# Optimization experiments

Hardware: AMD Instinct MI355X
Metric: run time of the kernel (lower is better)

The kernel has to match this reference:

```python
import jax, jax.numpy as jnp
import numpy as np

D_MODEL = 1024
NUM_HEADS = 16
HEAD_DIM = D_MODEL // NUM_HEADS


def setup_inputs() -> dict:
    key = jax.random.key(0)
    k_x, k_wqkv, k_bqkv, k_wfc, k_bfc = jax.random.split(key, 5)
    scale_in = 1.0 / np.sqrt(D_MODEL)
    return {
        "x": jax.random.normal(k_x, (2, 2048, D_MODEL), dtype=jnp.float32),
        # torch nn.Linear stores weight as [out_features, in_features]
        "w_qkv": jax.random.uniform(k_wqkv, (3 * D_MODEL, D_MODEL), jnp.float32, -scale_in, scale_in),
        "b_qkv": jax.random.uniform(k_bqkv, (3 * D_MODEL,), jnp.float32, -scale_in, scale_in),
        "w_fc": jax.random.uniform(k_wfc, (D_MODEL, D_MODEL), jnp.float32, -scale_in, scale_in),
        "b_fc": jax.random.uniform(k_bfc, (D_MODEL,), jnp.float32, -scale_in, scale_in),
    }


def reference(x, w_qkv, b_qkv, w_fc, b_fc):
    B, S, _ = x.shape
    # fused QKV projection: [B,S,3*d_model]
    qkv = jnp.einsum("bsd,ed->bse", x, w_qkv) + b_qkv
    # [B,S,H,3*head_dim] -> [B,H,S,3*head_dim]
    qkv = qkv.reshape(B, S, NUM_HEADS, 3 * HEAD_DIM).transpose(0, 2, 1, 3)
    Q, K, V = jnp.split(qkv, 3, axis=-1)  # each [B,H,S,head_dim]
    scores = jnp.einsum("bhqd,bhkd->bhqk", Q, K) / np.sqrt(HEAD_DIM).astype(np.float32)
    attention = jax.nn.softmax(scores, axis=-1)  # [B,H,S,S]
    values = jnp.einsum("bhqk,bhkd->bhqd", attention, V)
    # [B,H,S,head_dim] -> [B,S,d_model]
    values = values.transpose(0, 2, 1, 3).reshape(B, S, D_MODEL)
    out = jnp.einsum("bsd,ed->bse", values, w_fc) + b_fc
    return out
```

## Files before the change

### kernel.cpp

```cpp
#include <hip/hip_runtime.h>
#include <hip/hip_bf16.h>
#include <hip/hip_fp16.h>

#define D_MODEL 1024
#define NH 16
#define HD 64
#define BATCH 2
#define SEQ 2048

typedef __attribute__((ext_vector_type(8))) short short8;
typedef __attribute__((ext_vector_type(4))) float floatx4;
typedef __attribute__((ext_vector_type(16))) float floatx16;
typedef __attribute__((ext_vector_type(8))) _Float16 half8;

static __device__ __forceinline__ short f2bf(float f) {
    __hip_bfloat16 h = __float2bfloat16(f);
    return *reinterpret_cast<short*>(&h);
}
static __device__ __forceinline__ unsigned int pk2bf(float a, float b) {
    float2 t; t.x = a; t.y = b;
    __hip_bfloat162 h2 = __float22bfloat162_rn(t);
    return *reinterpret_cast<unsigned int*>(&h2);
}
static __device__ __forceinline__ void pl32swap(unsigned &a, unsigned &b) {
    asm("v_permlane32_swap_b32 %0, %1" : "+v"(a), "+v"(b));
}
static __device__ __forceinline__ short8 mk8(unsigned a, unsigned b,
                                             unsigned c, unsigned d) {
    union { unsigned u[4]; short8 s; } t;
    t.u[0] = a; t.u[1] = b; t.u[2] = c; t.u[3] = d;
    return t.s;
}

#define GLDS(gp, lp) __builtin_amdgcn_global_load_lds( \
    (const __attribute__((address_space(1))) void*)(gp), \
    (__attribute__((address_space(3))) void*)(lp), 16, 0, 0)

__global__ __launch_bounds__(256) void cvt_all(
    const float* __restrict__ x, const float* __restrict__ wq,
    const float* __restrict__ wf,
    short* __restrict__ Xb, short* __restrict__ Wqb, short* __restrict__ Wfb)
{
    int i = blockIdx.x * 256 + threadIdx.x;
    const float* src; short* dst; int off;
    if (i < 524288)      { src = x;  dst = Xb;  off = i; }
    else if (i < 917504) { src = wq; dst = Wqb; off = i - 524288; }
    else                 { src = wf; dst = Wfb; off = i - 917504; }
    float4 a = *reinterpret_cast<const float4*>(src + off * 8);
    float4 b = *reinterpret_cast<const float4*>(src + off * 8 + 4);
    short8 o;
    o[0] = f2bf(a.x); o[1] = f2bf(a.y); o[2] = f2bf(a.z); o[3] = f2bf(a.w);
    o[4] = f2bf(b.x); o[5] = f2bf(b.y); o[6] = f2bf(b.z); o[7] = f2bf(b.w);
    *reinterpret_cast<short8*>(dst + off * 8) = o;
}

__global__ __launch_bounds__(256) void qkv_gemm(
    const short* __restrict__ X, const short* __restrict__ W,
    const float* __restrict__ bias,
    short* __restrict__ Qs, short* __restrict__ Ks, short* __restrict__ Vt_g)
{
    __shared__ __align__(16) short As[128 * 128];
    __shared__ __align__(16) short Bs[128 * 128];
    const int tid = threadIdx.x;

    const int lin = blockIdx.x;
    const int g = lin & 7;
    const int loc = lin >> 3;
    const int mi = loc / 3;
    const int j3 = loc - mi * 3;
    const int m0 = mi * 128;
    const int n0 = (g + 8 * j3) * 128;
    const int bi = m0 >> 11, sl0 = m0 & 2047;

    const int w = tid >> 6, lane = tid & 63;
    const int quad = lane >> 4, l15 = lane & 15;
    const int wm2 = w >> 1, wn2 = w & 1;

    const int rg = lane >> 3;
    const int sl = lane & 7;
    const int cg = sl ^ rg;

    floatx4 acc[4][4];
#pragma unroll
    for (int i = 0; i < 4; i++)
#pragma unroll
        for (int j = 0; j < 4; j++) acc[i][j] = (floatx4)0.0f;

    for (int k0 = 0; k0 < 1024; k0 += 128) {
        __syncthreads();
#pragma unroll
        for (int jj = 0; jj < 4; jj++) {
            int grp = w * 4 + jj;
            int r = grp * 8 + rg;
#pragma unroll
            for (int kh = 0; kh < 2; kh++) {
                GLDS(&X[(size_t)(m0 + r) * 1024 + k0 + kh * 64 + cg * 8],
                     &As[grp * 1024 + kh * 512]);
                GLDS(&W[(size_t)(n0 + r) * 1024 + k0 + kh * 64 + cg * 8],
                     &Bs[grp * 1024 + kh * 512]);
            }
        }
        __syncthreads();
#pragma unroll
        for (int kk = 0; kk < 4; kk++) {
            const int kw = kk * 32 + quad * 8;
            const int base = (kw >> 6) * 512 +
                             ((((kw & 63) >> 3) ^ (l15 & 7)) * 8);
            short8 a[4], b[4];
#pragma unroll
            for (int t = 0; t < 4; t++) {
                int ra = wm2 * 64 + t * 16 + l15;
                int rb = wn2 * 64 + t * 16 + l15;
                a[t] = *reinterpret_cast<const short8*>(
                    &As[(ra >> 3) * 1024 + (ra & 7) * 64 + base]);
                b[t] = *reinterpret_cast<const short8*>(
                    &Bs[(rb >> 3) * 1024 + (rb & 7) * 64 + base]);
            }
#pragma unroll
            for (int mt = 0; mt < 4; mt++)
#pragma unroll
                for (int nt = 0; nt < 4; nt++)
                    acc[mt][nt] = __builtin_amdgcn_mfma_f32_16x16x32_bf16(
                        a[mt], b[nt], acc[mt][nt], 0, 0, 0);
        }
    }

    __syncthreads();
    short* EA = &As[0];
    short* T  = &As[0];
#pragma unroll
    for (int half = 0; half < 2; half++) {
        const int colg0 = n0 + half * 64;
        const int h = colg0 / 192;
        const int t = (colg0 % 192) / 64;
        if (wn2 == half) {
#pragma unroll
            for (int nt = 0; nt < 4; nt++) {
                int jj = nt * 16 + l15;
                float bv = bias[colg0 + jj];
#pragma unroll
                for (int mt = 0; mt < 4; mt++) {
#pragma unroll
                    for (int r = 0; r < 4; r++) {
                        int ml = wm2 * 64 + mt * 16 + quad * 4 + r;
                        float v = acc[mt][nt][r] + bv;
                        if (t == 0) v *= 0.18033688f;
                        if (t < 2) EA[ml * 72 + jj] = f2bf(v);
                        else       T[jj * 136 + ml] = f2bf(v);
                    }
                }
            }
        }
        __syncthreads();
        if (t < 2) {
            short* dst = (t == 0) ? Qs : Ks;
#pragma unroll
            for (int i = 0; i < 4; i++) {
                int c = tid + i * 256;
                int row = c >> 3, ck = c & 7;
                uint4 u = *reinterpret_cast<const uint4*>(&EA[row * 72 + ck * 8]);
                *reinterpret_cast<uint4*>(
                    &dst[((size_t)(bi * NH + h) * SEQ + sl0 + row) * HD + ck * 8]) = u;
            }
        } else {
#pragma unroll
            for (int i = 0; i < 4; i++) {
                int c = tid + i * 256;
                int d = c >> 4, ck = c & 15;
                uint4 u = *reinterpret_cast<const uint4*>(&T[d * 136 + ck * 8]);
                *reinterpret_cast<uint4*>(
                    &Vt_g[((size_t)(bi * NH + h) * HD + d) * SEQ + sl0 + ck * 8]) = u;
            }
        }
        __syncthreads();
    }
}

__global__ __launch_bounds__(256, 2) void attn_kernel(
    const short* __restrict__ Qs, const short* __restrict__ Ks,
    const short* __restrict__ Vt_g,
    _Float16* __restrict__ Opart, float* __restrict__ lpart)
{
    __shared__ __align__(16) short Kl[2][32 * 64];
    __shared__ __align__(16) short Vl[2][32 * 64];

    const int tid = threadIdx.x;
    const int w = tid >> 6, lane = tid & 63;
    const int hi = lane >> 5, l31 = lane & 31;

    const int lin = blockIdx.x;
    const int xcd = lin & 7;
    const int j = lin >> 3;
    const int qb = j & 7;
    const int grp = xcd + 8 * (j >> 3);
    const int khalf = grp & 1;
    const int h = (grp >> 1) & 15;
    const int bi = grp >> 5;
    const int bh = bi * NH + h;
    const int kbase = bh * SEQ * HD;
    const int vbase = bh * HD * SEQ;
    const int kt0 = khalf * (SEQ / 2);
    const int qw = qb * 256 + w * 64;

    const int sr = tid >> 3;
    const int ss = tid & 7;
    const int cgs = ss ^ (sr & 7);
    const short* kg = Ks + kbase + (size_t)(kt0 + sr) * HD + cgs * 8;
    const short* vg = Vt_g + vbase +
                      (size_t)(sr + (cgs >> 2) * 32) * SEQ + kt0 + (cgs & 3) * 8;

    const short8 onesv = {(short)0x3F80, (short)0x3F80, (short)0x3F80, (short)0x3F80,
                          (short)0x3F80, (short)0x3F80, (short)0x3F80, (short)0x3F80};

    short8 aq[2][4];
#pragma unroll
    for (int qt = 0; qt < 2; qt++) {
        const short* qp = Qs + kbase + (size_t)(qw + qt * 32 + l31) * HD + hi * 8;
#pragma unroll
        for (int c = 0; c < 4; c++)
            aq[qt][c] = *reinterpret_cast<const short8*>(qp + c * 16);
    }

    floatx16 o[2][2], ol[2];
#pragma unroll
    for (int qt = 0; qt < 2; qt++) {
        ol[qt] = (floatx16)0.0f;
        o[qt][0] = (floatx16)0.0f;
        o[qt][1] = (floatx16)0.0f;
    }

    const int rbase = (l31 >> 3) * 512 + (l31 & 7) * 64;
    const int rx = l31 & 7;

    GLDS(kg, &Kl[0][tid * 8]);
    GLDS(vg, &Vl[0][tid * 8]);
    __syncthreads();

    int cur = 0;
    for (int it = 0; it < SEQ / 2 / 32; it++) {
        GLDS(kg + (size_t)(it + 1) * (32 * HD), &Kl[cur ^ 1][tid * 8]);
        GLDS(vg + (it + 1) * 32, &Vl[cur ^ 1][tid * 8]);

        const short* Kb = &Kl[cur][0];
        const short* Vb = &Vl[cur][0];
        short8 kf[4], vA0, vA1, vB0, vB1;
#pragma unroll
        for (int c = 0; c < 4; c++)
            kf[c] = *reinterpret_cast<const short8*>(
                Kb + rbase + (((2 * c + hi) ^ rx) * 8));
        vA0 = *reinterpret_cast<const short8*>(Vb + rbase + (((0 + hi) ^ rx) * 8));
        vA1 = *reinterpret_cast<const short8*>(Vb + rbase + (((2 + hi) ^ rx) * 8));
        vB0 = *reinterpret_cast<const short8*>(Vb + rbase + (((4 + hi) ^ rx) * 8));
        vB1 = *reinterpret_cast<const short8*>(Vb + rbase + (((6 + hi) ^ rx) * 8));

#pragma unroll
        for (int qt = 0; qt < 2; qt++) {
            floatx16 s = (floatx16)0.0f;
            s = __builtin_amdgcn_mfma_f32_32x32x16_bf16(kf[0], aq[qt][0], s, 0, 0, 0);
            s = __builtin_amdgcn_mfma_f32_32x32x16_bf16(kf[1], aq[qt][1], s, 0, 0, 0);
            s = __builtin_amdgcn_mfma_f32_32x32x16_bf16(kf[2], aq[qt][2], s, 0, 0, 0);
            s = __builtin_amdgcn_mfma_f32_32x32x16_bf16(kf[3], aq[qt][3], s, 0, 0, 0);

            float p[16];
#pragma unroll
            for (int r = 0; r < 16; r++) p[r] = exp2f(s[r]);

            unsigned d0a = pk2bf(p[0], p[1]),   d2a = pk2bf(p[4], p[5]);
            unsigned d1a = pk2bf(p[2], p[3]),   d3a = pk2bf(p[6], p[7]);
            pl32swap(d0a, d2a);
            pl32swap(d1a, d3a);
            unsigned d0b = pk2bf(p[8], p[9]),   d2b = pk2bf(p[12], p[13]);
            unsigned d1b = pk2bf(p[10], p[11]), d3b = pk2bf(p[14], p[15]);
            pl32swap(d0b, d2b);
            pl32swap(d1b, d3b);
            short8 pa0 = mk8(d0a, d1a, d2a, d3a);
            short8 pa1 = mk8(d0b, d1b, d2b, d3b);

            o[qt][0] = __builtin_amdgcn_mfma_f32_32x32x16_bf16(pa0, vA0, o[qt][0], 0, 0, 0);
            o[qt][1] = __builtin_amdgcn_mfma_f32_32x32x16_bf16(pa0, vB0, o[qt][1], 0, 0, 0);
            o[qt][0] = __builtin_amdgcn_mfma_f32_32x32x16_bf16(pa1, vA1, o[qt][0], 0, 0, 0);
            o[qt][1] = __builtin_amdgcn_mfma_f32_32x32x16_bf16(pa1, vB1, o[qt][1], 0, 0, 0);
            ol[qt] = __builtin_amdgcn_mfma_f32_32x32x16_bf16(pa0, onesv, ol[qt], 0, 0, 0);
            ol[qt] = __builtin_amdgcn_mfma_f32_32x32x16_bf16(pa1, onesv, ol[qt], 0, 0, 0);
        }

        __syncthreads();
        cur ^= 1;
    }

#pragma unroll
    for (int qt = 0; qt < 2; qt++) {
#pragma unroll
        for (int r = 0; r < 16; r++) {
            int ql = qw + qt * 32 + (r & 3) + 8 * (r >> 2) + 4 * hi;
            size_t base = (size_t)khalf * (4096u * 1024u) +
                          ((size_t)bi * SEQ + ql) * D_MODEL + h * HD;
            Opart[base + l31]      = (_Float16)o[qt][0][r];
            Opart[base + 32 + l31] = (_Float16)o[qt][1][r];
            if (l31 == 0)
                lpart[khalf * 65536 + bh * SEQ + ql] = ol[qt][r];
        }
    }
}

__global__ __launch_bounds__(256) void combine_kernel(
    const _Float16* __restrict__ O, const float* __restrict__ lp,
    short* __restrict__ attnb)
{
    int i = blockIdx.x * 256 + threadIdx.x;
    int m = i >> 7;
    int e0 = (i & 127) * 8;
    int bi = m >> 11, s = m & 2047, h = e0 >> 6;
    int bh = bi * NH + h;
    float l = lp[bh * SEQ + s] + lp[65536 + bh * SEQ + s];
    float rl = 1.0f / l;
    size_t off = (size_t)m * D_MODEL + e0;
    half8 a = *reinterpret_cast<const half8*>(O + off);
    half8 b = *reinterpret_cast<const half8*>(O + 4096u * 1024u + off);
    short8 out;
#pragma unroll
    for (int j = 0; j < 8; j++)
        out[j] = f2bf(((float)a[j] + (float)b[j]) * rl);
    *reinterpret_cast<short8*>(attnb + off) = out;
}

__global__ __launch_bounds__(256) void fc_gemm(
    const short* __restrict__ A, const short* __restrict__ W,
    const float* __restrict__ bias, float* __restrict__ out)
{
    __shared__ __align__(16) short As[128 * 64];
    __shared__ __align__(16) short Bs[64 * 64];
    const int tid = threadIdx.x;
    const int m0 = blockIdx.y * 128;
    const int n0 = blockIdx.x * 64;
    const int w = tid >> 6, lane = tid & 63;
    const int quad = lane >> 4, l15 = lane & 15;
    const int wm2 = w >> 1, wn2 = w & 1;

    const int rg = lane >> 3;
    const int sl = lane & 7;
    const int cg = sl ^ rg;

    floatx4 acc[4][2];
#pragma unroll
    for (int i = 0; i < 4; i++)
#pragma unroll
        for (int j = 0; j < 2; j++) acc[i][j] = (floatx4)0.0f;

    for (int k0 = 0; k0 < 1024; k0 += 64) {
        __syncthreads();
#pragma unroll
        for (int j = 0; j < 4; j++) {
            int g = w * 4 + j;
            int r = g * 8 + rg;
            GLDS(&A[(size_t)(m0 + r) * 1024 + k0 + cg * 8], &As[g * 512]);
        }
#pragma unroll
        for (int j = 0; j < 2; j++) {
            int g = w * 2 + j;
            int r = g * 8 + rg;
            GLDS(&W[(size_t)(n0 + r) * 1024 + k0 + cg * 8], &Bs[g * 512]);
        }
        __syncthreads();
#pragma unroll
        for (int kk = 0; kk < 2; kk++) {
            int swz = ((kk * 4 + quad) ^ (l15 & 7)) * 8;
            short8 a[4], b[2];
#pragma unroll
            for (int i = 0; i < 4; i++)
                a[i] = *reinterpret_cast<const short8*>(
                    &As[(wm2 * 64 + i * 16 + l15) * 64 + swz]);
#pragma unroll
            for (int j = 0; j < 2; j++)
                b[j] = *reinterpret_cast<const short8*>(
                    &Bs[(wn2 * 32 + j * 16 + l15) * 64 + swz]);
#pragma unroll
            for (int mt = 0; mt < 4; mt++)
#pragma unroll
                for (int nt = 0; nt < 2; nt++)
                    acc[mt][nt] = __builtin_amdgcn_mfma_f32_16x16x32_bf16(
                        a[mt], b[nt], acc[mt][nt], 0, 0, 0);
        }
    }

#pragma unroll
    for (int nt = 0; nt < 2; nt++) {
        int col = n0 + wn2 * 32 + nt * 16 + l15;
        float bv = bias[col];
#pragma unroll
        for (int mt = 0; mt < 4; mt++) {
#pragma unroll
            for (int r = 0; r < 4; r++) {
                int row = m0 + wm2 * 64 + mt * 16 + quad * 4 + r;
                out[row * 1024 + col] = acc[mt][nt][r] + bv;
            }
        }
    }
}

extern "C" void kernel_launch(void* const* d_in, const int* in_sizes, int n_in,
                              void* d_out, int out_size, void* d_ws, size_t ws_size,
                              hipStream_t stream) {
    const float* x     = (const float*)d_in[0];
    const float* w_qkv = (const float*)d_in[1];
    const float* b_qkv = (const float*)d_in[2];
    const float* w_fc  = (const float*)d_in[3];
    const float* b_fc  = (const float*)d_in[4];
    float* out = (float*)d_out;

    const size_t M1 = 1024u * 1024u;
    short* ws = (short*)d_ws;
    short* Qs    = ws;
    short* Ks    = ws + 4 * M1;
    short* Vt_g  = ws + 8 * M1;
    short* Wfb   = ws + 12 * M1;
    short* Xb    = ws + 13 * M1;
    short* Wqb   = ws + 17 * M1;
    _Float16* Opart = (_Float16*)(ws + 13 * M1);
    float* lpart = (float*)(ws + 21 * M1);
    short* attnb = Qs;

    cvt_all<<<4096, 256, 0, stream>>>(x, w_qkv, w_fc, Xb, Wqb, Wfb);
    qkv_gemm<<<768, 256, 0, stream>>>(Xb, Wqb, b_qkv, Qs, Ks, Vt_g);
    attn_kernel<<<512, 256, 0, stream>>>(Qs, Ks, Vt_g, Opart, lpart);
    combine_kernel<<<2048, 256, 0, stream>>>(Opart, lpart, attnb);
    fc_gemm<<<dim3(16, 32), 256, 0, stream>>>(attnb, Wfb, b_fc, out);
}
```

Before: 214.5 us.

## Use 8 waves per attention block with one query tile each, sum rowsums on VALU

The attention kernel now launches 512 threads per block, with each wave handling one 32-row query tile instead of two. The K and V staging loads are split between the two halves of the block. The softmax row-sum is now accumulated with VALU adds plus a cross-half shuffle, replacing the extra MFMA against a ones vector. This cuts per-wave register pressure to allow more resident waves and removes two MFMAs per tile. In exchange, each wave now reuses the K/V fragments it reads from LDS for only one query tile.

Measured after the change: 213.7 us. About the same (-0.4%).

```diff
diff --git a/kernel.cpp b/kernel.cpp
--- a/kernel.cpp
+++ b/kernel.cpp
@@ -176,7 +176,7 @@
     }
 }
 
-__global__ __launch_bounds__(256, 2) void attn_kernel(
+__global__ __launch_bounds__(512, 4) void attn_kernel(
     const short* __restrict__ Qs, const short* __restrict__ Ks,
     const short* __restrict__ Vt_g,
     _Float16* __restrict__ Opart, float* __restrict__ lpart)
@@ -185,7 +185,8 @@
     __shared__ __align__(16) short Vl[2][32 * 64];
 
     const int tid = threadIdx.x;
-    const int w = tid >> 6, lane = tid & 63;
+    const int w = tid >> 6;
+    const int lane = tid & 63;
     const int hi = lane >> 5, l31 = lane & 31;
 
     const int lin = blockIdx.x;
@@ -200,46 +201,38 @@
     const int kbase = bh * SEQ * HD;
     const int vbase = bh * HD * SEQ;
     const int kt0 = khalf * (SEQ / 2);
-    const int qw = qb * 256 + w * 64;
-
-    const int sr = tid >> 3;
-    const int ss = tid & 7;
+    const int qw = qb * 256 + w * 32;
+
+    const int st = tid & 255;
+    const int sr = st >> 3;
+    const int ss = st & 7;
     const int cgs = ss ^ (sr & 7);
     const short* kg = Ks + kbase + (size_t)(kt0 + sr) * HD + cgs * 8;
     const short* vg = Vt_g + vbase +
                       (size_t)(sr + (cgs >> 2) * 32) * SEQ + kt0 + (cgs & 3) * 8;
 
-    const short8 onesv = {(short)0x3F80, (short)0x3F80, (short)0x3F80, (short)0x3F80,
-                          (short)0x3F80, (short)0x3F80, (short)0x3F80, (short)0x3F80};
-
-    short8 aq[2][4];
-#pragma unroll
-    for (int qt = 0; qt < 2; qt++) {
-        const short* qp = Qs + kbase + (size_t)(qw + qt * 32 + l31) * HD + hi * 8;
+    short8 aq[4];
+    {
+        const short* qp = Qs + kbase + (size_t)(qw + l31) * HD + hi * 8;
 #pragma unroll
         for (int c = 0; c < 4; c++)
-            aq[qt][c] = *reinterpret_cast<const short8*>(qp + c * 16);
-    }
-
-    floatx16 o[2][2], ol[2];
-#pragma unroll
-    for (int qt = 0; qt < 2; qt++) {
-        ol[qt] = (floatx16)0.0f;
-        o[qt][0] = (floatx16)0.0f;
-        o[qt][1] = (floatx16)0.0f;
-    }
+            aq[c] = *reinterpret_cast<const short8*>(qp + c * 16);
+    }
+
+    floatx16 o0 = (floatx16)0.0f, o1 = (floatx16)0.0f;
+    float l_acc = 0.0f;
 
     const int rbase = (l31 >> 3) * 512 + (l31 & 7) * 64;
     const int rx = l31 & 7;
 
-    GLDS(kg, &Kl[0][tid * 8]);
-    GLDS(vg, &Vl[0][tid * 8]);
+    if (tid < 256) GLDS(kg, &Kl[0][st * 8]);
+    else           GLDS(vg, &Vl[0][st * 8]);
     __syncthreads();
 
     int cur = 0;
     for (int it = 0; it < SEQ / 2 / 32; it++) {
-        GLDS(kg + (size_t)(it + 1) * (32 * HD), &Kl[cur ^ 1][tid * 8]);
-        GLDS(vg + (it + 1) * 32, &Vl[cur ^ 1][tid * 8]);
+        if (tid < 256) GLDS(kg + (size_t)(it + 1) * (32 * HD), &Kl[cur ^ 1][st * 8]);
+        else           GLDS(vg + (it + 1) * 32, &Vl[cur ^ 1][st * 8]);
 
         const short* Kb = &Kl[cur][0];
         const short* Vb = &Vl[cur][0];
@@ -253,54 +246,55 @@
         vB0 = *reinterpret_cast<const short8*>(Vb + rbase + (((4 + hi) ^ rx) * 8));
         vB1 = *reinterpret_cast<const short8*>(Vb + rbase + (((6 + hi) ^ rx) * 8));
 
-#pragma unroll
-        for (int qt = 0; qt < 2; qt++) {
-            floatx16 s = (floatx16)0.0f;
-            s = __builtin_amdgcn_mfma_f32_32x32x16_bf16(kf[0], aq[qt][0], s, 0, 0, 0);
-            s = __builtin_amdgcn_mfma_f32_32x32x16_bf16(kf[1], aq[qt][1], s, 0, 0, 0);
-            s = __builtin_amdgcn_mfma_f32_32x32x16_bf16(kf[2], aq[qt][2], s, 0, 0, 0);
-            s = __builtin_amdgcn_mfma_f32_32x32x16_bf16(kf[3], aq[qt][3], s, 0, 0, 0);
-
-            float p[16];
-#pragma unroll
-            for (int r = 0; r < 16; r++) p[r] = exp2f(s[r]);
-
-            unsigned d0a = pk2bf(p[0], p[1]),   d2a = pk2bf(p[4], p[5]);
-            unsigned d1a = pk2bf(p[2], p[3]),   d3a = pk2bf(p[6], p[7]);
-            pl32swap(d0a, d2a);
-            pl32swap(d1a, d3a);
-            unsigned d0b = pk2bf(p[8], p[9]),   d2b = pk2bf(p[12], p[13]);
-            unsigned d1b = pk2bf(p[10], p[11]), d3b = pk2bf(p[14], p[15]);
-            pl32swap(d0b, d2b);
-            pl32swap(d1b, d3b);
-            short8 pa0 = mk8(d0a, d1a, d2a, d3a);
-            short8 pa1 = mk8(d0b, d1b, d2b, d3b);
-
-            o[qt][0] = __builtin_amdgcn_mfma_f32_32x32x16_bf16(pa0, vA0, o[qt][0], 0, 0, 0);
-            o[qt][1] = __builtin_amdgcn_mfma_f32_32x32x16_bf16(pa0, vB0, o[qt][1], 0, 0, 0);
-            o[qt][0] = __builtin_amdgcn_mfma_f32_32x32x16_bf16(pa1, vA1, o[qt][0], 0, 0, 0);
-            o[qt][1] = __builtin_amdgcn_mfma_f32_32x32x16_bf16(pa1, vB1, o[qt][1], 0, 0, 0);
-            ol[qt] = __builtin_amdgcn_mfma_f32_32x32x16_bf16(pa0, onesv, ol[qt], 0, 0, 0);
-            ol[qt] = __builtin_amdgcn_mfma_f32_32x32x16_bf16(pa1, onesv, ol[qt], 0, 0, 0);
-        }
+        floatx16 s = (floatx16)0.0f;
+        s = __builtin_amdgcn_mfma_f32_32x32x16_bf16(kf[0], aq[0], s, 0, 0, 0);
+        s = __builtin_amdgcn_mfma_f32_32x32x16_bf16(kf[1], aq[1], s, 0, 0, 0);
+        s = __builtin_amdgcn_mfma_f32_32x32x16_bf16(kf[2], aq[2], s, 0, 0, 0);
+        s = __builtin_amdgcn_mfma_f32_32x32x16_bf16(kf[3], aq[3], s, 0, 0, 0);
+
+        float p[16];
+#pragma unroll
+        for (int r = 0; r < 16; r++) p[r] = exp2f(s[r]);
+
+        {
+            float s0 = (p[0] + p[1]) + (p[2] + p[3]);
+            float s1 = (p[4] + p[5]) + (p[6] + p[7]);
+            float s2 = (p[8] + p[9]) + (p[10] + p[11]);
+            float s3 = (p[12] + p[13]) + (p[14] + p[15]);
+            l_acc += (s0 + s1) + (s2 + s3);
+        }
+
+        unsigned d0a = pk2bf(p[0], p[1]),   d2a = pk2bf(p[4], p[5]);
+        unsigned d1a = pk2bf(p[2], p[3]),   d3a = pk2bf(p[6], p[7]);
+        pl32swap(d0a, d2a);
+        pl32swap(d1a, d3a);
+        unsigned d0b = pk2bf(p[8], p[9]),   d2b = pk2bf(p[12], p[13]);
+        unsigned d1b = pk2bf(p[10], p[11]), d3b = pk2bf(p[14], p[15]);
+        pl32swap(d0b, d2b);
+        pl32swap(d1b, d3b);
+        short8 pa0 = mk8(d0a, d1a, d2a, d3a);
+        short8 pa1 = mk8(d0b, d1b, d2b, d3b);
+
+        o0 = __builtin_amdgcn_mfma_f32_32x32x16_bf16(pa0, vA0, o0, 0, 0, 0);
+        o1 = __builtin_amdgcn_mfma_f32_32x32x16_bf16(pa0, vB0, o1, 0, 0, 0);
+        o0 = __builtin_amdgcn_mfma_f32_32x32x16_bf16(pa1, vA1, o0, 0, 0, 0);
+        o1 = __builtin_amdgcn_mfma_f32_32x32x16_bf16(pa1, vB1, o1, 0, 0, 0);
 
         __syncthreads();
         cur ^= 1;
     }
 
 #pragma unroll
-    for (int qt = 0; qt < 2; qt++) {
-#pragma unroll
-        for (int r = 0; r < 16; r++) {
-            int ql = qw + qt * 32 + (r & 3) + 8 * (r >> 2) + 4 * hi;
-            size_t base = (size_t)khalf * (4096u * 1024u) +
-                          ((size_t)bi * SEQ + ql) * D_MODEL + h * HD;
-            Opart[base + l31]      = (_Float16)o[qt][0][r];
-            Opart[base + 32 + l31] = (_Float16)o[qt][1][r];
-            if (l31 == 0)
-                lpart[khalf * 65536 + bh * SEQ + ql] = ol[qt][r];
-        }
-    }
+    for (int r = 0; r < 16; r++) {
+        int ql = qw + (r & 3) + 8 * (r >> 2) + 4 * hi;
+        size_t base = (size_t)khalf * (4096u * 1024u) +
+                      ((size_t)bi * SEQ + ql) * D_MODEL + h * HD;
+        Opart[base + l31]      = (_Float16)o0[r];
+        Opart[base + 32 + l31] = (_Float16)o1[r];
+    }
+    float l_oth = __shfl_xor(l_acc, 32);
+    if (hi == 0)
+        lpart[khalf * 65536 + bh * SEQ + qw + l31] = l_acc + l_oth;
 }
 
 __global__ __launch_bounds__(256) void combine_kernel(
@@ -422,7 +416,7 @@
 
     cvt_all<<<4096, 256, 0, stream>>>(x, w_qkv, w_fc, Xb, Wqb, Wfb);
     qkv_gemm<<<768, 256, 0, stream>>>(Xb, Wqb, b_qkv, Qs, Ks, Vt_g);
-    attn_kernel<<<512, 256, 0, stream>>>(Qs, Ks, Vt_g, Opart, lpart);
+    attn_kernel<<<512, 512, 0, stream>>>(Qs, Ks, Vt_g, Opart, lpart);
     combine_kernel<<<2048, 256, 0, stream>>>(Opart, lpart, attnb);
     fc_gemm<<<dim3(16, 32), 256, 0, stream>>>(attnb, Wfb, b_fc, out);
 }
```
